# Kernel tuning notes

Hardware: AMD Instinct MI355X
Metric: run time of the kernel (lower is better)

## Reference

```python
import jax, jax.numpy as jnp
import numpy as np

ROUTE_SCALE = 2.5
TOP_K = 2
N_EXPERTS = 16


def setup_inputs() -> dict:
    key = jax.random.key(0)
    ks = jax.random.split(key, 8)
    B, T, D, I, E = 2, 1024, 768, 384, N_EXPERTS
    s = 0.02
    return {
        "x": jax.random.normal(ks[0], (B, T, D), dtype=jnp.float32),
        "gate_w": jax.random.normal(ks[1], (E, D), dtype=jnp.float32) * s,
        "sg_w": jax.random.normal(ks[2], (I, D), dtype=jnp.float32) * s,
        "su_w": jax.random.normal(ks[3], (I, D), dtype=jnp.float32) * s,
        "sd_w": jax.random.normal(ks[4], (D, I), dtype=jnp.float32) * s,
        "rg_w": jax.random.normal(ks[5], (E, I, D), dtype=jnp.float32) * s,
        "ru_w": jax.random.normal(ks[6], (E, I, D), dtype=jnp.float32) * s,
        "rd_w": jax.random.normal(ks[7], (E, D, I), dtype=jnp.float32) * s,
    }


def _moe_forward(x, gate_w, sg_w, su_w, sd_w, rg_w, ru_w, rd_w):
    B, T, D = x.shape
    flat = x.reshape(-1, D)  # (N, D), N = B*T

    # ---- shared expert (SwiGLU FFN) ----
    g = flat @ sg_w.T
    u = flat @ su_w.T
    shared_out = (jax.nn.silu(g) * u) @ sd_w.T  # (N, D)

    # ---- gate: softmax(fp32) -> top-k -> renormalize ----
    logits = (flat @ gate_w.T) * ROUTE_SCALE  # (N, E)
    scores = jax.nn.softmax(logits.astype(jnp.float32), axis=-1)
    topk_w, topk_i = jax.lax.top_k(scores, TOP_K)  # (N, K)
    topk_w = topk_w / jnp.sum(topk_w, axis=-1, keepdims=True)
    topk_w = topk_w.astype(x.dtype)

    # aux load-balancing loss
    one_hot = jax.nn.one_hot(topk_i, N_EXPERTS, dtype=jnp.float32)  # (N, K, E)
    mask = one_hot.sum(axis=1)  # (N, E)
    f = mask.mean(axis=0)
    p = scores.mean(axis=0)
    aux_loss = jnp.sum(f * p) * N_EXPERTS

    # combine weights per (token, expert): sum_k w_k * [idx_k == e]
    combine = jnp.einsum("nk,nke->ne", topk_w, one_hot.astype(x.dtype))  # (N, E)

    # ---- routed experts as batched (grouped) SwiGLU GEMMs ----
    rg = jnp.einsum("nd,eid->nei", flat, rg_w)  # (N, E, I)
    ru = jnp.einsum("nd,eid->nei", flat, ru_w)
    rh = jax.nn.silu(rg) * ru  # (N, E, I)
    eo = jnp.einsum("nei,edi->ned", rh, rd_w)  # (N, E, D)
    routed_out = jnp.einsum("ned,ne->nd", eo, combine)  # (N, D)

    out = (shared_out + routed_out).reshape(B, T, D)
    return out, aux_loss


def reference(x, gate_w, sg_w, su_w, sd_w, rg_w, ru_w, rd_w):
    return _moe_forward(x, gate_w, sg_w, su_w, sd_w, rg_w, ru_w, rd_w)
```

## Files before the change

kernel.cpp:

```cpp
#include <hip/hip_runtime.h>
#include <math.h>

#define NTOK 2048
#define DDIM 768
#define IDIM 384
#define NEXP 16
#define ECAP 2048
#define HSHARED (NEXP * ECAP)
#define GBLK (NTOK / 4)

#define MT 64
#define NSHT2 32
#define NRT2 80
#define NW2 ((NSHT2 + NRT2) * 6)
#define CH2 (NW2 / 8)
#define KH 384
#define XS2_LD 392
#define HS_LD 392

#define ZBLK 1536
#define CBLK (768 + 288 * 17 + 144 * 17)

typedef __attribute__((ext_vector_type(8))) short short8;
typedef __attribute__((ext_vector_type(4))) float f32x4;

__device__ __forceinline__ unsigned short f2bf(float f) {
    unsigned int u = __float_as_uint(f);
    unsigned int r = (u + 0x7fffu + ((u >> 16) & 1u)) >> 16;
    return (unsigned short)r;
}

#define WS_XB   1048576u
#define WS_W1F  4194304u
#define WS_WDF  24248320u
#define WS_H    34275328u

__global__ __launch_bounds__(256) void gate_kernel(
    const float* __restrict__ x, const float* __restrict__ gate_w,
    int* __restrict__ topk_i, float* __restrict__ topk_w,
    float* __restrict__ p_partial) {
    __shared__ float p_blk[16];
    int tid = threadIdx.x;
    if (tid < 16) p_blk[tid] = 0.f;
    __syncthreads();

    int wave = tid >> 6, lane = tid & 63;
    int n = blockIdx.x * 4 + wave;
    int e = lane >> 2, q = lane & 3;
    const float4* xr = (const float4*)(x + (size_t)n * DDIM);
    const float4* wr = (const float4*)(gate_w + (size_t)e * DDIM);
    float s = 0.f;
    #pragma unroll 4
    for (int k = q * 48; k < q * 48 + 48; ++k) {
        float4 a = xr[k], b = wr[k];
        s += a.x * b.x + a.y * b.y + a.z * b.z + a.w * b.w;
    }
    s += __shfl_xor(s, 1);
    s += __shfl_xor(s, 2);
    float logit = s * 2.5f;

    float m = logit;
    #pragma unroll
    for (int mask = 4; mask < 64; mask <<= 1)
        m = fmaxf(m, __shfl_xor(m, mask));
    float ex = __expf(logit - m);
    float sum = ex;
    #pragma unroll
    for (int mask = 4; mask < 64; mask <<= 1)
        sum += __shfl_xor(sum, mask);
    float sc = ex / sum;

    float v = sc; int idx = e;
    #pragma unroll
    for (int mask = 4; mask < 64; mask <<= 1) {
        float ov = __shfl_xor(v, mask);
        int   oi = __shfl_xor(idx, mask);
        if (ov > v || (ov == v && oi < idx)) { v = ov; idx = oi; }
    }
    float b0 = v; int i0 = idx;
    v = (e == i0) ? -1.f : sc; idx = e;
    #pragma unroll
    for (int mask = 4; mask < 64; mask <<= 1) {
        float ov = __shfl_xor(v, mask);
        int   oi = __shfl_xor(idx, mask);
        if (ov > v || (ov == v && oi < idx)) { v = ov; idx = oi; }
    }
    float b1 = v; int i1 = idx;
    float rs = 1.f / (b0 + b1);

    if (lane == 0) {
        topk_i[n * 2] = i0; topk_i[n * 2 + 1] = i1;
        topk_w[n * 2] = b0 * rs; topk_w[n * 2 + 1] = b1 * rs;
    }
    if (q == 0) atomicAdd(&p_blk[e], sc);
    __syncthreads();
    if (tid < 16) p_partial[blockIdx.x * 16 + tid] = p_blk[tid];
}

__global__ __launch_bounds__(256) void convzero_kernel(
    const float* __restrict__ x,
    const float* __restrict__ rgw, const float* __restrict__ ruw,
    const float* __restrict__ sgw, const float* __restrict__ suw,
    const float* __restrict__ rdw, const float* __restrict__ sdw,
    float4* __restrict__ out4,
    unsigned short* __restrict__ xb, unsigned short* __restrict__ w1f,
    unsigned short* __restrict__ wdf) {
    int b = blockIdx.x, tid = threadIdx.x;

    if (b < ZBLK) {
        int i = b * 256 + tid;
        if (i < NTOK * DDIM / 4) out4[i] = make_float4(0.f, 0.f, 0.f, 0.f);
        return;
    }
    b -= ZBLK;

    const float* s;
    unsigned short* dst;
    if (b < 768) {
        int i = b * 256 + tid;
        s = x + (size_t)i * 8;
        dst = xb + (size_t)i * 8;
    } else if (b < 768 + 288 * 17) {
        int bb = b - 768;
        int E = bb / 288, bx = bb % 288;
        const float* gsrc = (E == 16) ? sgw : rgw + (size_t)E * (IDIM * DDIM);
        const float* usrc = (E == 16) ? suw : ruw + (size_t)E * (IDIM * DDIM);
        int i = bx * 256 + tid;
        int lane = i & 63;
        int fi = i >> 6;
        int ks = fi % 24, rg = fi / 24;
        int b16 = rg >> 1, gu = rg & 1;
        s = (gu ? usrc : gsrc)
          + (size_t)(b16 * 16 + (lane & 15)) * DDIM + ks * 32 + (lane >> 4) * 8;
        dst = w1f + (size_t)E * (DDIM * DDIM) + (size_t)i * 8;
    } else {
        int bb = b - (768 + 288 * 17);
        int E = bb / 144, bx = bb % 144;
        const float* src = (E == 16) ? sdw : rdw + (size_t)E * (DDIM * IDIM);
        int i = bx * 256 + tid;
        int lane = i & 63;
        int fi = i >> 6;
        int ks = fi % 12, cg = fi / 12;
        s = src + (size_t)(cg * 16 + (lane & 15)) * IDIM + ks * 32 + (lane >> 4) * 8;
        dst = wdf + (size_t)E * (DDIM * IDIM) + (size_t)i * 8;
    }
    float4 v0 = *(const float4*)s, v1 = *(const float4*)(s + 4);
    short8 o;
    o[0]=f2bf(v0.x); o[1]=f2bf(v0.y); o[2]=f2bf(v0.z); o[3]=f2bf(v0.w);
    o[4]=f2bf(v1.x); o[5]=f2bf(v1.y); o[6]=f2bf(v1.z); o[7]=f2bf(v1.w);
    *(short8*)dst = o;
}

__global__ __launch_bounds__(256) void route_kernel(
    const int* __restrict__ topk_i, const float* __restrict__ topk_w,
    const float* __restrict__ p_partial,
    int* __restrict__ counts, int* __restrict__ perm_t, float* __restrict__ perm_w,
    float* __restrict__ out_aux) {
    __shared__ float s_p[256];
    __shared__ float s_psum[16];
    __shared__ int s_cnt[16];
    __shared__ int s_cur[16];
    int tid = threadIdx.x;
    {
        int e = tid & 15, g = tid >> 4;
        float acc = 0.f;
        for (int b = g; b < GBLK; b += 16) acc += p_partial[b * 16 + e];
        s_p[tid] = acc;
    }
    if (tid < 16) { s_cnt[tid] = 0; s_cur[tid] = 0; }
    __syncthreads();
    if (tid < 16) {
        float a = 0.f;
        #pragma unroll
        for (int g = 0; g < 16; ++g) a += s_p[g * 16 + tid];
        s_psum[tid] = a;
    }
    for (int n = tid; n < NTOK; n += 256) {
        atomicAdd(&s_cnt[topk_i[n * 2]], 1);
        atomicAdd(&s_cnt[topk_i[n * 2 + 1]], 1);
    }
    __syncthreads();
    if (tid < 16) counts[tid] = s_cnt[tid];
    if (tid == 0) {
        float a = 0.f;
        for (int e = 0; e < 16; ++e) a += (float)s_cnt[e] * s_psum[e];
        out_aux[0] = a * 16.f / ((float)NTOK * (float)NTOK);
    }
    for (int n = tid; n < NTOK; n += 256) {
        #pragma unroll
        for (int k = 0; k < 2; ++k) {
            int e = topk_i[n * 2 + k];
            int pos = atomicAdd(&s_cur[e], 1);
            perm_t[e * ECAP + pos] = n;
            perm_w[e * ECAP + pos] = topk_w[n * 2 + k];
        }
    }
}

__device__ __forceinline__ void swz_decode(int lid, int& bx, int& y) {
    int wid = (lid & 7) * CH2 + (lid >> 3);
    bx = wid / 6;
    y = wid - bx * 6;
}

__device__ __forceinline__ bool tile_decode(const int* __restrict__ counts,
                                            int r, int& e, int& t, int& cnt) {
    int acc = 0;
    for (int ee = 0; ee < NEXP; ++ee) {
        int c = counts[ee];
        int tiles = (c + 63) >> 6;
        if (r < acc + tiles) { e = ee; t = r - acc; cnt = c; return true; }
        acc += tiles;
    }
    return false;
}

__global__ __launch_bounds__(256, 3) void p1_kernel(
    const unsigned short* __restrict__ xb, const unsigned short* __restrict__ w1f,
    const int* __restrict__ counts, const int* __restrict__ perm_t,
    unsigned short* __restrict__ h) {
    __shared__ unsigned short xs[MT * XS2_LD];
    __shared__ int s_tok[MT];

    int tid = threadIdx.x;
    int bx, y;
    swz_decode(blockIdx.x, bx, y);
    int e, hbase;
    if (bx < NSHT2) {
        e = 16;
        hbase = HSHARED + bx * MT;
        if (tid < MT) s_tok[tid] = bx * MT + tid;
    } else {
        int t, cnt;
        if (!tile_decode(counts, bx - NSHT2, e, t, cnt)) return;
        hbase = e * ECAP + t * MT;
        if (tid < MT) {
            int slot = t * MT + tid;
            s_tok[tid] = (slot < cnt) ? perm_t[e * ECAP + slot] : 0;
        }
    }
    __syncthreads();

    int lane = tid & 63, wave = tid >> 6;
    int lr = lane & 15, kg = (lane >> 4) * 8, jrow = (lane >> 4) * 4;

    const unsigned short* pg = w1f + ((((size_t)e * 48 + (y * 8 + wave * 2    )) * 24) * 64 + lane) * 8;
    const unsigned short* pu = w1f + ((((size_t)e * 48 + (y * 8 + wave * 2 + 1)) * 24) * 64 + lane) * 8;

    f32x4 ag0 = (f32x4)0.f, ag1 = (f32x4)0.f, ag2 = (f32x4)0.f, ag3 = (f32x4)0.f;
    f32x4 au0 = (f32x4)0.f, au1 = (f32x4)0.f, au2 = (f32x4)0.f, au3 = (f32x4)0.f;

    #pragma unroll
    for (int half = 0; half < 2; ++half) {
        if (half) __syncthreads();
        for (int c = tid; c < MT * 48; c += 256) {
            int row = c / 48, off = (c - row * 48) * 8;
            *(short8*)(xs + row * XS2_LD + off) =
                *(const short8*)(xb + (size_t)s_tok[row] * DDIM + half * KH + off);
        }
        __syncthreads();

        for (int ks = 0; ks < 12; ++ks) {
            int ksg = half * 12 + ks;
            short8 bg = *(const short8*)(pg + (size_t)ksg * 512);
            short8 bu = *(const short8*)(pu + (size_t)ksg * 512);
            short8 a0 = *(const short8*)(xs + (     lr) * XS2_LD + ks * 32 + kg);
            short8 a1 = *(const short8*)(xs + (16 + lr) * XS2_LD + ks * 32 + kg);
            short8 a2 = *(const short8*)(xs + (32 + lr) * XS2_LD + ks * 32 + kg);
            short8 a3 = *(const short8*)(xs + (48 + lr) * XS2_LD + ks * 32 + kg);
            ag0 = __builtin_amdgcn_mfma_f32_16x16x32_bf16(a0, bg, ag0, 0, 0, 0);
            au0 = __builtin_amdgcn_mfma_f32_16x16x32_bf16(a0, bu, au0, 0, 0, 0);
            ag1 = __builtin_amdgcn_mfma_f32_16x16x32_bf16(a1, bg, ag1, 0, 0, 0);
            au1 = __builtin_amdgcn_mfma_f32_16x16x32_bf16(a1, bu, au1, 0, 0, 0);
            ag2 = __builtin_amdgcn_mfma_f32_16x16x32_bf16(a2, bg, ag2, 0, 0, 0);
            au2 = __builtin_amdgcn_mfma_f32_16x16x32_bf16(a2, bu, au2, 0, 0, 0);
            ag3 = __builtin_amdgcn_mfma_f32_16x16x32_bf16(a3, bg, ag3, 0, 0, 0);
            au3 = __builtin_amdgcn_mfma_f32_16x16x32_bf16(a3, bu, au3, 0, 0, 0);
        }
    }

    int colg = y * 64 + wave * 16 + lr;
    #pragma unroll
    for (int mf = 0; mf < 4; ++mf) {
        f32x4 g4 = (mf == 0) ? ag0 : (mf == 1) ? ag1 : (mf == 2) ? ag2 : ag3;
        f32x4 u4 = (mf == 0) ? au0 : (mf == 1) ? au1 : (mf == 2) ? au2 : au3;
        #pragma unroll
        for (int j = 0; j < 4; ++j) {
            int tl = mf * 16 + jrow + j;
            float g = g4[j], u = u4[j];
            float hv = g / (1.f + __expf(-g)) * u;
            h[(size_t)(hbase + tl) * IDIM + colg] = f2bf(hv);
        }
    }
}

__global__ __launch_bounds__(256, 3) void p2_kernel(
    const unsigned short* __restrict__ h, const unsigned short* __restrict__ wdf,
    const int* __restrict__ counts,
    const int* __restrict__ perm_t, const float* __restrict__ perm_w,
    float* __restrict__ out) {
    __shared__ unsigned short hs[MT * HS_LD];
    __shared__ int   s_tok[MT];
    __shared__ float s_w[MT];

    int tid = threadIdx.x;
    int bx, y;
    swz_decode(blockIdx.x, bx, y);
    int e, hbase;
    if (bx < NSHT2) {
        e = 16;
        hbase = HSHARED + bx * MT;
        if (tid < MT) { s_tok[tid] = bx * MT + tid; s_w[tid] = 1.f; }
    } else {
        int t, cnt;
        if (!tile_decode(counts, bx - NSHT2, e, t, cnt)) return;
        hbase = e * ECAP + t * MT;
        if (tid < MT) {
            int slot = t * MT + tid;
            bool v = slot < cnt;
            s_tok[tid] = v ? perm_t[e * ECAP + slot] : 0;
            s_w[tid]   = v ? perm_w[e * ECAP + slot] : 0.f;
        }
    }
    __syncthreads();

    for (int c = tid; c < MT * 48; c += 256) {
        int row = c / 48, off = (c - row * 48) * 8;
        *(short8*)(hs + row * HS_LD + off) =
            *(const short8*)(h + (size_t)(hbase + row) * IDIM + off);
    }
    __syncthreads();

    int lane = tid & 63, wave = tid >> 6;
    int lr = lane & 15, kg = (lane >> 4) * 8, jrow = (lane >> 4) * 4;

    const unsigned short* p0 = wdf + ((((size_t)e * 48 + (y * 8 + wave * 2    )) * 12) * 64 + lane) * 8;
    const unsigned short* p1 = wdf + ((((size_t)e * 48 + (y * 8 + wave * 2 + 1)) * 12) * 64 + lane) * 8;

    f32x4 c00 = (f32x4)0.f, c01 = (f32x4)0.f, c02 = (f32x4)0.f, c03 = (f32x4)0.f;
    f32x4 c10 = (f32x4)0.f, c11 = (f32x4)0.f, c12 = (f32x4)0.f, c13 = (f32x4)0.f;
    for (int ks = 0; ks < 12; ++ks) {
        short8 b0 = *(const short8*)(p0 + (size_t)ks * 512);
        short8 b1 = *(const short8*)(p1 + (size_t)ks * 512);
        short8 a0 = *(const short8*)(hs + (     lr) * HS_LD + ks * 32 + kg);
        short8 a1 = *(const short8*)(hs + (16 + lr) * HS_LD + ks * 32 + kg);
        short8 a2 = *(const short8*)(hs + (32 + lr) * HS_LD + ks * 32 + kg);
        short8 a3 = *(const short8*)(hs + (48 + lr) * HS_LD + ks * 32 + kg);
        c00 = __builtin_amdgcn_mfma_f32_16x16x32_bf16(a0, b0, c00, 0, 0, 0);
        c10 = __builtin_amdgcn_mfma_f32_16x16x32_bf16(a0, b1, c10, 0, 0, 0);
        c01 = __builtin_amdgcn_mfma_f32_16x16x32_bf16(a1, b0, c01, 0, 0, 0);
        c11 = __builtin_amdgcn_mfma_f32_16x16x32_bf16(a1, b1, c11, 0, 0, 0);
        c02 = __builtin_amdgcn_mfma_f32_16x16x32_bf16(a2, b0, c02, 0, 0, 0);
        c12 = __builtin_amdgcn_mfma_f32_16x16x32_bf16(a2, b1, c12, 0, 0, 0);
        c03 = __builtin_amdgcn_mfma_f32_16x16x32_bf16(a3, b0, c03, 0, 0, 0);
        c13 = __builtin_amdgcn_mfma_f32_16x16x32_bf16(a3, b1, c13, 0, 0, 0);
    }

    int col0 = y * 128 + wave * 32 + lr;
    #pragma unroll
    for (int mf = 0; mf < 4; ++mf) {
        f32x4 v0 = (mf == 0) ? c00 : (mf == 1) ? c01 : (mf == 2) ? c02 : c03;
        f32x4 v1 = (mf == 0) ? c10 : (mf == 1) ? c11 : (mf == 2) ? c12 : c13;
        #pragma unroll
        for (int j = 0; j < 4; ++j) {
            int tl = mf * 16 + jrow + j;
            float w = s_w[tl];
            if (w == 0.f) continue;
            float* orow = out + (size_t)s_tok[tl] * DDIM;
            atomicAdd(orow + col0,      w * v0[j]);
            atomicAdd(orow + col0 + 16, w * v1[j]);
        }
    }
}

extern "C" void kernel_launch(void* const* d_in, const int* in_sizes, int n_in,
                              void* d_out, int out_size, void* d_ws, size_t ws_size,
                              hipStream_t stream) {
    const float* x      = (const float*)d_in[0];
    const float* gate_w = (const float*)d_in[1];
    const float* sg_w   = (const float*)d_in[2];
    const float* su_w   = (const float*)d_in[3];
    const float* sd_w   = (const float*)d_in[4];
    const float* rg_w   = (const float*)d_in[5];
    const float* ru_w   = (const float*)d_in[6];
    const float* rd_w   = (const float*)d_in[7];
    float* out = (float*)d_out;

    char* ws = (char*)d_ws;
    int*   counts    = (int*)(ws + 0);
    int*   perm_t    = (int*)(ws + 1024);
    float* perm_w    = (float*)(ws + 132096);
    float* p_partial = (float*)(ws + 263168);
    int*   topk_i    = (int*)(ws + 295936);
    float* topk_w    = (float*)(ws + 312320);
    unsigned short* xb  = (unsigned short*)(ws + WS_XB);
    unsigned short* w1f = (unsigned short*)(ws + WS_W1F);
    unsigned short* wdf = (unsigned short*)(ws + WS_WDF);
    unsigned short* hbuf= (unsigned short*)(ws + WS_H);

    gate_kernel<<<GBLK, 256, 0, stream>>>(x, gate_w, topk_i, topk_w, p_partial);

    convzero_kernel<<<ZBLK + CBLK, 256, 0, stream>>>(
        x, rg_w, ru_w, sg_w, su_w, rd_w, sd_w,
        (float4*)out, xb, w1f, wdf);

    route_kernel<<<1, 256, 0, stream>>>(topk_i, topk_w, p_partial,
                                        counts, perm_t, perm_w,
                                        out + (size_t)NTOK * DDIM);

    p1_kernel<<<NW2, 256, 0, stream>>>(xb, w1f, counts, perm_t, hbuf);

    p2_kernel<<<NW2, 256, 0, stream>>>(hbuf, wdf, counts, perm_t, perm_w, out);
}
```

Measured before the change: 103.5 us.

## Use direct global-to-LDS loads in fragment layout and batch convert blocks

The p1 and p2 kernels now stage activation tiles with global_load_lds 16-byte transfers, writing straight into an MFMA-fragment-ordered LDS layout so each lane reads its A operand contiguously. This removes the register round-trip and the padded row layout. The convert/zero kernel also processes four chunks per block, which cuts the block count fourfold. The fragment layout depends on each wave loading its own 16 rows, and the per-lane reads must line up with that layout.

Result: no change. 101.8 us (-1.7%).

```diff
diff --git a/kernel.cpp b/kernel.cpp
--- a/kernel.cpp
+++ b/kernel.cpp
@@ -15,11 +15,12 @@
 #define NW2 ((NSHT2 + NRT2) * 6)
 #define CH2 (NW2 / 8)
 #define KH 384
-#define XS2_LD 392
-#define HS_LD 392
-
-#define ZBLK 1536
-#define CBLK (768 + 288 * 17 + 144 * 17)
+
+#define ZBLK4 384
+#define XBLK4 192
+#define W1BLK4 (72 * 17)
+#define WDBLK4 (36 * 17)
+#define CZBLK (ZBLK4 + XBLK4 + W1BLK4 + WDBLK4)
 
 typedef __attribute__((ext_vector_type(8))) short short8;
 typedef __attribute__((ext_vector_type(4))) float f32x4;
@@ -28,6 +29,12 @@
     unsigned int u = __float_as_uint(f);
     unsigned int r = (u + 0x7fffu + ((u >> 16) & 1u)) >> 16;
     return (unsigned short)r;
+}
+
+__device__ __forceinline__ void gload16(const void* g, void* l) {
+    __builtin_amdgcn_global_load_lds(
+        (const __attribute__((address_space(1))) void*)g,
+        (__attribute__((address_space(3))) void*)l, 16, 0, 0);
 }
 
 #define WS_XB   1048576u
@@ -107,48 +114,73 @@
     unsigned short* __restrict__ wdf) {
     int b = blockIdx.x, tid = threadIdx.x;
 
-    if (b < ZBLK) {
-        int i = b * 256 + tid;
-        if (i < NTOK * DDIM / 4) out4[i] = make_float4(0.f, 0.f, 0.f, 0.f);
+    if (b < ZBLK4) {
+        float4 z = make_float4(0.f, 0.f, 0.f, 0.f);
+        float4* dst = out4 + b * 1024 + tid;
+        #pragma unroll
+        for (int j = 0; j < 4; ++j) dst[j * 256] = z;
         return;
     }
-    b -= ZBLK;
-
-    const float* s;
-    unsigned short* dst;
-    if (b < 768) {
-        int i = b * 256 + tid;
-        s = x + (size_t)i * 8;
-        dst = xb + (size_t)i * 8;
-    } else if (b < 768 + 288 * 17) {
-        int bb = b - 768;
-        int E = bb / 288, bx = bb % 288;
+    b -= ZBLK4;
+
+    if (b < XBLK4) {
+        #pragma unroll
+        for (int j = 0; j < 4; ++j) {
+            int i = b * 1024 + j * 256 + tid;
+            const float* s = x + (size_t)i * 8;
+            float4 v0 = *(const float4*)s, v1 = *(const float4*)(s + 4);
+            short8 o;
+            o[0]=f2bf(v0.x); o[1]=f2bf(v0.y); o[2]=f2bf(v0.z); o[3]=f2bf(v0.w);
+            o[4]=f2bf(v1.x); o[5]=f2bf(v1.y); o[6]=f2bf(v1.z); o[7]=f2bf(v1.w);
+            *(short8*)(xb + (size_t)i * 8) = o;
+        }
+        return;
+    }
+    b -= XBLK4;
+
+    if (b < W1BLK4) {
+        int E = b / 72, bx = b % 72;
         const float* gsrc = (E == 16) ? sgw : rgw + (size_t)E * (IDIM * DDIM);
         const float* usrc = (E == 16) ? suw : ruw + (size_t)E * (IDIM * DDIM);
-        int i = bx * 256 + tid;
-        int lane = i & 63;
-        int fi = i >> 6;
-        int ks = fi % 24, rg = fi / 24;
-        int b16 = rg >> 1, gu = rg & 1;
-        s = (gu ? usrc : gsrc)
-          + (size_t)(b16 * 16 + (lane & 15)) * DDIM + ks * 32 + (lane >> 4) * 8;
-        dst = w1f + (size_t)E * (DDIM * DDIM) + (size_t)i * 8;
-    } else {
-        int bb = b - (768 + 288 * 17);
-        int E = bb / 144, bx = bb % 144;
+        unsigned short* wbase = w1f + (size_t)E * (DDIM * DDIM);
+        #pragma unroll
+        for (int j = 0; j < 4; ++j) {
+            int i = bx * 1024 + j * 256 + tid;
+            int lane = i & 63;
+            int fi = i >> 6;
+            int ks = fi % 24, rg = fi / 24;
+            int b16 = rg >> 1, gu = rg & 1;
+            const float* s = (gu ? usrc : gsrc)
+              + (size_t)(b16 * 16 + (lane & 15)) * DDIM + ks * 32 + (lane >> 4) * 8;
+            float4 v0 = *(const float4*)s, v1 = *(const float4*)(s + 4);
+            short8 o;
+            o[0]=f2bf(v0.x); o[1]=f2bf(v0.y); o[2]=f2bf(v0.z); o[3]=f2bf(v0.w);
+            o[4]=f2bf(v1.x); o[5]=f2bf(v1.y); o[6]=f2bf(v1.z); o[7]=f2bf(v1.w);
+            *(short8*)(wbase + (size_t)i * 8) = o;
+        }
+        return;
+    }
+    b -= W1BLK4;
+
+    {
+        int E = b / 36, bx = b % 36;
         const float* src = (E == 16) ? sdw : rdw + (size_t)E * (DDIM * IDIM);
-        int i = bx * 256 + tid;
-        int lane = i & 63;
-        int fi = i >> 6;
-        int ks = fi % 12, cg = fi / 12;
-        s = src + (size_t)(cg * 16 + (lane & 15)) * IDIM + ks * 32 + (lane >> 4) * 8;
-        dst = wdf + (size_t)E * (DDIM * IDIM) + (size_t)i * 8;
-    }
-    float4 v0 = *(const float4*)s, v1 = *(const float4*)(s + 4);
-    short8 o;
-    o[0]=f2bf(v0.x); o[1]=f2bf(v0.y); o[2]=f2bf(v0.z); o[3]=f2bf(v0.w);
-    o[4]=f2bf(v1.x); o[5]=f2bf(v1.y); o[6]=f2bf(v1.z); o[7]=f2bf(v1.w);
-    *(short8*)dst = o;
+        unsigned short* wbase = wdf + (size_t)E * (DDIM * IDIM);
+        #pragma unroll
+        for (int j = 0; j < 4; ++j) {
+            int i = bx * 1024 + j * 256 + tid;
+            int lane = i & 63;
+            int fi = i >> 6;
+            int ks = fi % 12, cg = fi / 12;
+            const float* s = src
+              + (size_t)(cg * 16 + (lane & 15)) * IDIM + ks * 32 + (lane >> 4) * 8;
+            float4 v0 = *(const float4*)s, v1 = *(const float4*)(s + 4);
+            short8 o;
+            o[0]=f2bf(v0.x); o[1]=f2bf(v0.y); o[2]=f2bf(v0.z); o[3]=f2bf(v0.w);
+            o[4]=f2bf(v1.x); o[5]=f2bf(v1.y); o[6]=f2bf(v1.z); o[7]=f2bf(v1.w);
+            *(short8*)(wbase + (size_t)i * 8) = o;
+        }
+    }
 }
 
 __global__ __launch_bounds__(256) void route_kernel(
@@ -219,7 +251,7 @@
     const unsigned short* __restrict__ xb, const unsigned short* __restrict__ w1f,
     const int* __restrict__ counts, const int* __restrict__ perm_t,
     unsigned short* __restrict__ h) {
-    __shared__ unsigned short xs[MT * XS2_LD];
+    __shared__ unsigned short xs[48 * 512];
     __shared__ int s_tok[MT];
 
     int tid = threadIdx.x;
@@ -242,7 +274,9 @@
     __syncthreads();
 
     int lane = tid & 63, wave = tid >> 6;
-    int lr = lane & 15, kg = (lane >> 4) * 8, jrow = (lane >> 4) * 4;
+    int lr = lane & 15, kg8 = (lane >> 4) * 8, jrow = (lane >> 4) * 4;
+
+    const unsigned short* gsrc = xb + (size_t)s_tok[wave * 16 + lr] * DDIM + kg8;
 
     const unsigned short* pg = w1f + ((((size_t)e * 48 + (y * 8 + wave * 2    )) * 24) * 64 + lane) * 8;
     const unsigned short* pu = w1f + ((((size_t)e * 48 + (y * 8 + wave * 2 + 1)) * 24) * 64 + lane) * 8;
@@ -253,21 +287,19 @@
     #pragma unroll
     for (int half = 0; half < 2; ++half) {
         if (half) __syncthreads();
-        for (int c = tid; c < MT * 48; c += 256) {
-            int row = c / 48, off = (c - row * 48) * 8;
-            *(short8*)(xs + row * XS2_LD + off) =
-                *(const short8*)(xb + (size_t)s_tok[row] * DDIM + half * KH + off);
-        }
+        #pragma unroll
+        for (int c = 0; c < 12; ++c)
+            gload16(gsrc + half * KH + c * 32, &xs[(wave * 12 + c) * 512]);
         __syncthreads();
 
         for (int ks = 0; ks < 12; ++ks) {
             int ksg = half * 12 + ks;
             short8 bg = *(const short8*)(pg + (size_t)ksg * 512);
             short8 bu = *(const short8*)(pu + (size_t)ksg * 512);
-            short8 a0 = *(const short8*)(xs + (     lr) * XS2_LD + ks * 32 + kg);
-            short8 a1 = *(const short8*)(xs + (16 + lr) * XS2_LD + ks * 32 + kg);
-            short8 a2 = *(const short8*)(xs + (32 + lr) * XS2_LD + ks * 32 + kg);
-            short8 a3 = *(const short8*)(xs + (48 + lr) * XS2_LD + ks * 32 + kg);
+            short8 a0 = *(const short8*)(xs + (     ks) * 512 + lane * 8);
+            short8 a1 = *(const short8*)(xs + (12 + ks) * 512 + lane * 8);
+            short8 a2 = *(const short8*)(xs + (24 + ks) * 512 + lane * 8);
+            short8 a3 = *(const short8*)(xs + (36 + ks) * 512 + lane * 8);
             ag0 = __builtin_amdgcn_mfma_f32_16x16x32_bf16(a0, bg, ag0, 0, 0, 0);
             au0 = __builtin_amdgcn_mfma_f32_16x16x32_bf16(a0, bu, au0, 0, 0, 0);
             ag1 = __builtin_amdgcn_mfma_f32_16x16x32_bf16(a1, bg, ag1, 0, 0, 0);
@@ -299,7 +331,7 @@
     const int* __restrict__ counts,
     const int* __restrict__ perm_t, const float* __restrict__ perm_w,
     float* __restrict__ out) {
-    __shared__ unsigned short hs[MT * HS_LD];
+    __shared__ unsigned short hs[48 * 512];
     __shared__ int   s_tok[MT];
     __shared__ float s_w[MT];
 
@@ -324,15 +356,14 @@
     }
     __syncthreads();
 
-    for (int c = tid; c < MT * 48; c += 256) {
-        int row = c / 48, off = (c - row * 48) * 8;
-        *(short8*)(hs + row * HS_LD + off) =
-            *(const short8*)(h + (size_t)(hbase + row) * IDIM + off);
-    }
-    __syncthreads();
-
     int lane = tid & 63, wave = tid >> 6;
-    int lr = lane & 15, kg = (lane >> 4) * 8, jrow = (lane >> 4) * 4;
+    int lr = lane & 15, kg8 = (lane >> 4) * 8, jrow = (lane >> 4) * 4;
+
+    const unsigned short* gsrc = h + (size_t)(hbase + wave * 16 + lr) * IDIM + kg8;
+    #pragma unroll
+    for (int c = 0; c < 12; ++c)
+        gload16(gsrc + c * 32, &hs[(wave * 12 + c) * 512]);
+    __syncthreads();
 
     const unsigned short* p0 = wdf + ((((size_t)e * 48 + (y * 8 + wave * 2    )) * 12) * 64 + lane) * 8;
     const unsigned short* p1 = wdf + ((((size_t)e * 48 + (y * 8 + wave * 2 + 1)) * 12) * 64 + lane) * 8;
@@ -342,10 +373,10 @@
     for (int ks = 0; ks < 12; ++ks) {
         short8 b0 = *(const short8*)(p0 + (size_t)ks * 512);
         short8 b1 = *(const short8*)(p1 + (size_t)ks * 512);
-        short8 a0 = *(const short8*)(hs + (     lr) * HS_LD + ks * 32 + kg);
-        short8 a1 = *(const short8*)(hs + (16 + lr) * HS_LD + ks * 32 + kg);
-        short8 a2 = *(const short8*)(hs + (32 + lr) * HS_LD + ks * 32 + kg);
-        short8 a3 = *(const short8*)(hs + (48 + lr) * HS_LD + ks * 32 + kg);
+        short8 a0 = *(const short8*)(hs + (     ks) * 512 + lane * 8);
+        short8 a1 = *(const short8*)(hs + (12 + ks) * 512 + lane * 8);
+        short8 a2 = *(const short8*)(hs + (24 + ks) * 512 + lane * 8);
+        short8 a3 = *(const short8*)(hs + (36 + ks) * 512 + lane * 8);
         c00 = __builtin_amdgcn_mfma_f32_16x16x32_bf16(a0, b0, c00, 0, 0, 0);
         c10 = __builtin_amdgcn_mfma_f32_16x16x32_bf16(a0, b1, c10, 0, 0, 0);
         c01 = __builtin_amdgcn_mfma_f32_16x16x32_bf16(a1, b0, c01, 0, 0, 0);
@@ -400,7 +431,7 @@
 
     gate_kernel<<<GBLK, 256, 0, stream>>>(x, gate_w, topk_i, topk_w, p_partial);
 
-    convzero_kernel<<<ZBLK + CBLK, 256, 0, stream>>>(
+    convzero_kernel<<<CZBLK, 256, 0, stream>>>(
         x, rg_w, ru_w, sg_w, su_w, rd_w, sd_w,
         (float4*)out, xb, w1f, wdf);
 
```
